# Kernel optimization log

Measured on AMD Instinct MI355X. Metric: run time of the kernel, lower is better.

## Reference

```python
import jax, jax.numpy as jnp
import numpy as np
import math

B, S, F_IN, D, H = 2048, 100, 158, 512, 8
HD = D // H  # head dim = 64


def _sinusoidal_pe(max_len, d_model):
    pos = np.arange(max_len, dtype=np.float32)[:, None]
    div = np.exp(np.arange(0, d_model, 2, dtype=np.float32) * (-math.log(10000.0) / d_model))
    pe = np.zeros((max_len, d_model), dtype=np.float32)
    pe[:, 0::2] = np.sin(pos * div)
    pe[:, 1::2] = np.cos(pos * div)
    return jnp.asarray(pe)


def setup_inputs() -> dict:
    key = jax.random.key(0)
    ks = jax.random.split(key, 16)
    s = 0.03  # small init scale to keep softmax well-conditioned
    return {
        "src": jax.random.normal(ks[0], (B, S, F_IN), jnp.float32),
        "W_feat": jax.random.normal(ks[1], (D, F_IN), jnp.float32) * s,
        "b_feat": jnp.zeros((D,), jnp.float32),
        "pe": _sinusoidal_pe(100, D),
        "Wq": jax.random.normal(ks[2], (D, D), jnp.float32) * s,
        "bq": jnp.zeros((D,), jnp.float32),
        "Wk": jax.random.normal(ks[3], (D, D), jnp.float32) * s,
        "bk": jnp.zeros((D,), jnp.float32),
        "Wv": jax.random.normal(ks[4], (D, D), jnp.float32) * s,
        "bv": jnp.zeros((D,), jnp.float32),
        "Wo": jax.random.normal(ks[5], (D, D), jnp.float32) * s,
        "bo": jnp.zeros((D,), jnp.float32),
        "ln_w": jnp.ones((D,), jnp.float32),
        "ln_b": jnp.zeros((D,), jnp.float32),
        "W1": jax.random.normal(ks[6], (F_IN, D), jnp.float32) * s,
        "b1": jnp.zeros((F_IN,), jnp.float32),
        "W2": jax.random.normal(ks[7], (D, F_IN), jnp.float32) * s,
        "b2": jnp.zeros((D,), jnp.float32),
        "Wt": jax.random.normal(ks[8], (D, D), jnp.float32) * s,
        "W_out": jax.random.normal(ks[9], (1, D), jnp.float32) * s,
        "b_out": jnp.zeros((1,), jnp.float32),
    }


def _layernorm(x, w, b, eps=1e-5):
    mu = jnp.mean(x, axis=-1, keepdims=True)
    var = jnp.var(x, axis=-1, keepdims=True)
    return (x - mu) * jax.lax.rsqrt(var + eps) * w + b


def reference(src, W_feat, b_feat, pe, Wq, bq, Wk, bk, Wv, bv, Wo, bo,
              ln_w, ln_b, W1, b1, W2, b2, Wt, W_out, b_out):
    # feature projection + sinusoidal PE  (dropout is identity in eval mode)
    x = src @ W_feat.T + b_feat            # [B,S,D]
    x = x + pe[:S]                          # [B,S,D]

    # naive multi-head attention
    def heads(t):  # [B,S,D] -> [B,H,S,HD]
        return t.reshape(B, S, H, HD).transpose(0, 2, 1, 3)
    q = heads(x @ Wq.T + bq)
    k = heads(x @ Wk.T + bk)
    v = heads(x @ Wv.T + bv)
    scores = jnp.einsum('bhqd,bhkd->bhqk', q, k) / jnp.sqrt(jnp.float32(HD))
    probs = jax.nn.softmax(scores, axis=-1)
    attn = jnp.einsum('bhqk,bhkd->bhqd', probs, v)
    attn = attn.transpose(0, 2, 1, 3).reshape(B, S, D)
    attn_out = attn @ Wo.T + bo

    # addnorm #1: x + LayerNorm(x) (note: residual is of the SAME tensor)
    y1 = attn_out + _layernorm(attn_out, ln_w, ln_b)

    # FFN (hidden = 158 per the code's d_ff reuse)
    ffn = jax.nn.relu(y1 @ W1.T + b1) @ W2.T + b2

    # addnorm #2 (same shared AddNormLayer params)
    y2 = ffn + _layernorm(ffn, ln_w, ln_b)

    # temporal attention pooling over time
    h = y2 @ Wt.T                           # [B,S,D]
    lam = jnp.einsum('bsd,bd->bs', h, h[:, -1, :])
    lam = jax.nn.softmax(lam, axis=1)
    pooled = jnp.einsum('bs,bsd->bd', lam, y2)  # [B,D]

    return pooled @ W_out.T + b_out         # [B,1]
```

## Files before the change

kernel.cpp:

```cpp
#include <hip/hip_runtime.h>
#include <math.h>

#define NB 2048
#define NS 100
#define NF 158
#define ND 512
#define NH 8

typedef unsigned short u16;
typedef __attribute__((ext_vector_type(8))) short bf16x8;
typedef __attribute__((ext_vector_type(8))) unsigned short u16x8;
typedef __attribute__((ext_vector_type(4))) float f32x4;

__device__ __forceinline__ u16 f2bf(float f) {
    union { float f; unsigned u; } v; v.f = f;
    unsigned u = v.u;
    return (u16)((u + 0x7fffu + ((u >> 16) & 1u)) >> 16);
}

__device__ __forceinline__ float bf2f(u16 v) {
    union { unsigned u; float f; } x; x.u = ((unsigned)v) << 16; return x.f;
}

__device__ __forceinline__ void gload16(const void* g, void* l) {
    __builtin_amdgcn_global_load_lds(
        (const __attribute__((address_space(1))) unsigned*)g,
        (__attribute__((address_space(3))) unsigned*)l, 16, 0, 0);
}

__device__ __forceinline__ bf16x8 load8_cvt(const float* __restrict__ base, int c0) {
    bf16x8 r;
    if (c0 + 8 <= NF) {
        #pragma unroll
        for (int j = 0; j < 8; j += 2) {
            float2 v = *(const float2*)(base + c0 + j);
            r[j] = (short)f2bf(v.x); r[j + 1] = (short)f2bf(v.y);
        }
    } else {
        #pragma unroll
        for (int j = 0; j < 8; ++j)
            r[j] = (c0 + j < NF) ? (short)f2bf(base[c0 + j]) : (short)0;
    }
    return r;
}

__global__ __launch_bounds__(256) void prep_w_kernel(
    const float* __restrict__ Wq, const float* __restrict__ Wk,
    const float* __restrict__ Wv, const float* __restrict__ Wfeat,
    u16* __restrict__ Wf)
{
    int bid = blockIdx.x;
    int sel = bid >> 9;
    int n = bid & 511;
    const float* Wsrc = (sel == 0) ? Wq : (sel == 1) ? Wk : Wv;
    __shared__ float wrow[ND];
    int t = threadIdx.x;
    wrow[t] = Wsrc[(size_t)n * ND + t];
    wrow[t + 256] = Wsrc[(size_t)n * ND + t + 256];
    __syncthreads();
    if (t < 160) {
        float acc = 0.f;
        if (t < NF)
            for (int d = 0; d < ND; ++d)
                acc += wrow[d] * Wfeat[(size_t)d * NF + t];
        int h = n >> 6, local = n & 63;
        int ni, l16;
        if (sel < 2) { ni = local & 3; l16 = local >> 2; }
        else         { ni = (local >> 4) & 3; l16 = local & 15; }
        int ks = t >> 5, quad = (t >> 3) & 3, j = t & 7;
        size_t idx = (((((size_t)sel * 8 + h) * 4 + ni) * 5 + ks) * 64
                      + (quad << 4) + l16) * 8 + j;
        Wf[idx] = f2bf(acc);
    }
}

__global__ __launch_bounds__(256) void prep_c_kernel(
    const float* __restrict__ Wq, const float* __restrict__ Wk, const float* __restrict__ Wv,
    const float* __restrict__ bq, const float* __restrict__ bk, const float* __restrict__ bv,
    const float* __restrict__ bfeat, const float* __restrict__ pe,
    float* __restrict__ T4)
{
    int bid = blockIdx.x;
    int sel = bid / 100;
    int s = bid - sel * 100;
    const float* Wsrc = (sel == 0) ? Wq : (sel == 1) ? Wk : Wv;
    const float* bsrc = (sel == 0) ? bq : (sel == 1) ? bk : bv;
    __shared__ float xv[ND];
    int t = threadIdx.x;
    xv[t] = bfeat[t] + pe[(size_t)s * ND + t];
    xv[t + 256] = bfeat[t + 256] + pe[(size_t)s * ND + t + 256];
    __syncthreads();
    #pragma unroll
    for (int rr = 0; rr < 2; ++rr) {
        int r = t + (rr << 8);
        const float* wr = Wsrc + (size_t)r * ND;
        float acc = bsrc[r];
        for (int d = 0; d < ND; d += 4) {
            float4 w4 = *(const float4*)(wr + d);
            acc += w4.x * xv[d] + w4.y * xv[d+1] + w4.z * xv[d+2] + w4.w * xv[d+3];
        }
        int h = r >> 6, local = r & 63;
        int idx64 = (sel < 2) ? local : (((local & 15) << 2) | (local >> 4));
        T4[(((size_t)(sel * 8 + h)) * 100 + s) * 64 + idx64] = acc;
    }
}

__global__ __launch_bounds__(256) void pad_cast_kernel(
    const float* __restrict__ src, u16* __restrict__ dst,
    int R, int C, int Cp, int total)
{
    int idx = blockIdx.x * 256 + threadIdx.x;
    if (idx >= total) return;
    int r = idx / Cp, c = idx - r * Cp;
    float v = (r < R && c < C) ? src[(size_t)r * C + c] : 0.f;
    dst[idx] = f2bf(v);
}

__global__ __launch_bounds__(256) void pad_b1_kernel(
    const float* __restrict__ b1, float* __restrict__ b1p)
{
    int t = threadIdx.x;
    b1p[t] = (t < NF) ? b1[t] : 0.f;
}

#define ALDQ 72
#define ALDP 136

__global__ __launch_bounds__(512, 4) void qkv_attn_kernel(
    const float* __restrict__ src, const u16* __restrict__ Wf,
    const float* __restrict__ T4, u16* __restrict__ O)
{
    __shared__ short UN[128 * ALDP];
    __shared__ short Ks[112 * ALDQ];
    __shared__ short Vt[64 * ALDP];

    int t = threadIdx.x;
    int lane = t & 63, wave = t >> 6;
    int quad = lane >> 4, l16 = lane & 15;
    int rows0 = wave << 4;
    int b = blockIdx.x;
    const float* xb = src + (size_t)b * NS * NF;
    const size_t rowbase = (size_t)b * NS;
    f32x4 z = {0.f, 0.f, 0.f, 0.f};

    for (int l = t; l < 12 * ALDQ; l += 512)
        Ks[(100 + l / ALDQ) * ALDQ + (l % ALDQ)] = 0;
    for (int l = t; l < 64 * 28; l += 512) {
        int d = l / 28, s = 100 + (l - d * 28);
        Vt[d * ALDP + s] = 0;
    }

    int arow = rows0 + l16;
    bf16x8 AF[5];
    {
        const float* xr = xb + (size_t)arow * NF;
        #pragma unroll
        for (int ks = 0; ks < 5; ++ks) {
            if (arow < NS) AF[ks] = load8_cvt(xr, (ks << 5) + (quad << 3));
            else { bf16x8 zz = {0,0,0,0,0,0,0,0}; AF[ks] = zz; }
        }
    }

    for (int h = 0; h < NH; ++h) {
        #pragma unroll
        for (int sel = 0; sel < 3; ++sel) {
            f32x4 acc[4];
            #pragma unroll
            for (int ni = 0; ni < 4; ++ni) acc[ni] = z;
            #pragma unroll
            for (int ks = 0; ks < 5; ++ks) {
                bf16x8 wfr[4];
                #pragma unroll
                for (int ni = 0; ni < 4; ++ni)
                    wfr[ni] = *(const bf16x8*)(Wf +
                        (((((size_t)sel * 8 + h) * 4 + ni) * 5 + ks) * 64 + lane) * 8);
                #pragma unroll
                for (int ni = 0; ni < 4; ++ni)
                    acc[ni] = __builtin_amdgcn_mfma_f32_16x16x32_bf16(
                        AF[ks], wfr[ni], acc[ni], 0, 0, 0);
            }
            #pragma unroll
            for (int r = 0; r < 4; ++r) {
                int row_s = rows0 + (quad << 2) + r;
                bool real = row_s < NS;
                float4 tv = make_float4(0.f, 0.f, 0.f, 0.f);
                if (real)
                    tv = *(const float4*)(T4 +
                        (((size_t)(sel * 8 + h)) * 100 + row_s) * 64 + (l16 << 2));
                if (sel < 2) {
                    ushort4 pk;
                    pk.x = f2bf(acc[0][r] + tv.x);
                    pk.y = f2bf(acc[1][r] + tv.y);
                    pk.z = f2bf(acc[2][r] + tv.z);
                    pk.w = f2bf(acc[3][r] + tv.w);
                    if (sel == 0) *(ushort4*)&UN[row_s * ALDP + (l16 << 2)] = pk;
                    else if (real) *(ushort4*)&Ks[row_s * ALDQ + (l16 << 2)] = pk;
                } else {
                    float tvs[4] = {tv.x, tv.y, tv.z, tv.w};
                    #pragma unroll
                    for (int ni = 0; ni < 4; ++ni) {
                        int nloc = (ni << 4) + l16;
                        float v = acc[ni][r] + tvs[ni];
                        if (real) Vt[nloc * ALDP + row_s] = (short)f2bf(v);
                    }
                }
            }
        }
        __syncthreads();

        f32x4 sc[7];
        #pragma unroll
        for (int ni = 0; ni < 7; ++ni) sc[ni] = z;
        #pragma unroll
        for (int ks = 0; ks < 2; ++ks) {
            bf16x8 aq = *(const bf16x8*)&UN[(rows0 + l16) * ALDP + (ks << 5) + (quad << 3)];
            bf16x8 bk[7];
            #pragma unroll
            for (int ni = 0; ni < 7; ++ni)
                bk[ni] = *(const bf16x8*)&Ks[((ni << 4) + l16) * ALDQ + (ks << 5) + (quad << 3)];
            #pragma unroll
            for (int ni = 0; ni < 7; ++ni)
                sc[ni] = __builtin_amdgcn_mfma_f32_16x16x32_bf16(aq, bk[ni], sc[ni], 0, 0, 0);
        }
        __syncthreads();

        #pragma unroll
        for (int r = 0; r < 4; ++r) {
            if (l16 >= 4) sc[6][r] = -3.0e38f;
            float mx = sc[0][r];
            #pragma unroll
            for (int ni = 1; ni < 7; ++ni) mx = fmaxf(mx, sc[ni][r]);
            #pragma unroll
            for (int off = 1; off < 16; off <<= 1) mx = fmaxf(mx, __shfl_xor(mx, off));
            float sum = 0.f;
            #pragma unroll
            for (int ni = 0; ni < 7; ++ni) {
                float e = expf((sc[ni][r] - mx) * 0.125f);
                sc[ni][r] = e; sum += e;
            }
            #pragma unroll
            for (int off = 1; off < 16; off <<= 1) sum += __shfl_xor(sum, off);
            float inv = 1.f / sum;
            int row = rows0 + (quad << 2) + r;
            #pragma unroll
            for (int ni = 0; ni < 7; ++ni)
                UN[row * ALDP + (ni << 4) + l16] = (short)f2bf(sc[ni][r] * inv);
            UN[row * ALDP + 112 + l16] = 0;
        }
        __syncthreads();

        f32x4 oa[4];
        #pragma unroll
        for (int ni = 0; ni < 4; ++ni) oa[ni] = z;
        #pragma unroll
        for (int ks = 0; ks < 4; ++ks) {
            bf16x8 ap = *(const bf16x8*)&UN[(rows0 + l16) * ALDP + (ks << 5) + (quad << 3)];
            bf16x8 bv[4];
            #pragma unroll
            for (int ni = 0; ni < 4; ++ni)
                bv[ni] = *(const bf16x8*)&Vt[((ni << 4) + l16) * ALDP + (ks << 5) + (quad << 3)];
            #pragma unroll
            for (int ni = 0; ni < 4; ++ni)
                oa[ni] = __builtin_amdgcn_mfma_f32_16x16x32_bf16(ap, bv[ni], oa[ni], 0, 0, 0);
        }
        #pragma unroll
        for (int r = 0; r < 4; ++r) {
            int row = rows0 + (quad << 2) + r;
            if (row < NS) {
                u16* orow = O + (rowbase + row) * 512 + (h << 6);
                #pragma unroll
                for (int ni = 0; ni < 4; ++ni)
                    orow[(ni << 4) + l16] = f2bf(oa[ni][r]);
            }
        }
        __syncthreads();
    }
}

template<int OUTMODE, bool RELU>
__global__ __launch_bounds__(256) void gemm_bf16(
    const u16* __restrict__ A, const u16* __restrict__ W,
    const float* __restrict__ bias, void* __restrict__ Cv, int K, int ldc)
{
    __shared__ short As[128 * 32];
    __shared__ short Bs[128 * 32];
    int t = threadIdx.x;
    int lane = t & 63, wave = t >> 6;
    int quad = lane >> 4, l16 = lane & 15;
    int wr = wave >> 1, wc = wave & 1;
    int m0 = blockIdx.y << 7, n0 = blockIdx.x << 7;

    f32x4 acc[4][4];
    f32x4 z = {0.f, 0.f, 0.f, 0.f};
    #pragma unroll
    for (int mi = 0; mi < 4; ++mi)
        #pragma unroll
        for (int ni = 0; ni < 4; ++ni) acc[mi][ni] = z;

    int rowA = t >> 2;
    int cch = (t & 3) << 3;
    const u16* aSrc0 = A + (size_t)(m0 + rowA) * K + cch;
    const u16* aSrc1 = A + (size_t)(m0 + rowA + 64) * K + cch;
    const u16* bSrc0 = W + (size_t)(n0 + rowA) * K + cch;
    const u16* bSrc1 = W + (size_t)(n0 + rowA + 64) * K + cch;
    short* aDst0 = As + t * 8;
    short* aDst1 = As + (t + 256) * 8;
    short* bDst0 = Bs + t * 8;
    short* bDst1 = Bs + (t + 256) * 8;

    int nk = K >> 5;
    for (int kc = 0; kc < nk; ++kc) {
        if (kc) __syncthreads();
        gload16(aSrc0, aDst0);
        gload16(aSrc1, aDst1);
        gload16(bSrc0, bDst0);
        gload16(bSrc1, bDst1);
        aSrc0 += 32; aSrc1 += 32; bSrc0 += 32; bSrc1 += 32;
        __syncthreads();

        bf16x8 af[4], bw[4];
        #pragma unroll
        for (int mi = 0; mi < 4; ++mi)
            af[mi] = *(const bf16x8*)(As + ((size_t)((wr << 6) + (mi << 4) + l16) * 32 + (quad << 3)));
        #pragma unroll
        for (int ni = 0; ni < 4; ++ni)
            bw[ni] = *(const bf16x8*)(Bs + ((size_t)((wc << 6) + (ni << 4) + l16) * 32 + (quad << 3)));
        #pragma unroll
        for (int mi = 0; mi < 4; ++mi)
            #pragma unroll
            for (int ni = 0; ni < 4; ++ni)
                acc[mi][ni] = __builtin_amdgcn_mfma_f32_16x16x32_bf16(af[mi], bw[ni], acc[mi][ni], 0, 0, 0);
    }

    #pragma unroll
    for (int mi = 0; mi < 4; ++mi) {
        #pragma unroll
        for (int r = 0; r < 4; ++r) {
            int row = m0 + (wr << 6) + (mi << 4) + (quad << 2) + r;
            #pragma unroll
            for (int ni = 0; ni < 4; ++ni) {
                int col = n0 + (wc << 6) + (ni << 4) + l16;
                float v = acc[mi][ni][r];
                if (bias) v += bias[col];
                if (RELU) v = fmaxf(v, 0.f);
                if (OUTMODE == 0)
                    ((float*)Cv)[(size_t)row * ldc + col] = v;
                else
                    ((u16*)Cv)[(size_t)row * ldc + col] = f2bf(v);
            }
        }
    }
}

template<int OUTMODE>
__global__ __launch_bounds__(512, 2) void gemm_ln(
    const u16* __restrict__ A, const u16* __restrict__ W,
    const float* __restrict__ bias, const float* __restrict__ lnw,
    const float* __restrict__ lnb, void* __restrict__ outv, int K)
{
    __shared__ short As[64 * 32];
    __shared__ short Bs[512 * 32];
    __shared__ float red_s[64][9];
    __shared__ float red_q[64][9];
    __shared__ float mrow[64], rrow[64];

    int t = threadIdx.x;
    int lane = t & 63, wave = t >> 6;
    int quad = lane >> 4, l16 = lane & 15;
    int m0 = blockIdx.x << 6;

    f32x4 acc[4][4];
    f32x4 z = {0.f, 0.f, 0.f, 0.f};
    #pragma unroll
    for (int mi = 0; mi < 4; ++mi)
        #pragma unroll
        for (int ni = 0; ni < 4; ++ni) acc[mi][ni] = z;

    int koff = (t & 3) << 3;
    const u16* aSrc = A + (size_t)(m0 + (t >> 2)) * K + koff;
    const u16* bSrc0 = W + (size_t)(t >> 2) * K + koff;
    const u16* bSrc1 = W + (size_t)((t >> 2) + 128) * K + koff;
    const u16* bSrc2 = W + (size_t)((t >> 2) + 256) * K + koff;
    const u16* bSrc3 = W + (size_t)((t >> 2) + 384) * K + koff;
    short* aDst = As + t * 8;
    short* bDst0 = Bs + t * 8;
    short* bDst1 = Bs + (t + 512) * 8;
    short* bDst2 = Bs + (t + 1024) * 8;
    short* bDst3 = Bs + (t + 1536) * 8;

    int nk = K >> 5;
    for (int kc = 0; kc < nk; ++kc) {
        if (kc) __syncthreads();
        if (t < 256) gload16(aSrc, aDst);
        gload16(bSrc0, bDst0);
        gload16(bSrc1, bDst1);
        gload16(bSrc2, bDst2);
        gload16(bSrc3, bDst3);
        aSrc += 32; bSrc0 += 32; bSrc1 += 32; bSrc2 += 32; bSrc3 += 32;
        __syncthreads();

        bf16x8 af[4], bw[4];
        #pragma unroll
        for (int mi = 0; mi < 4; ++mi)
            af[mi] = *(const bf16x8*)(As + ((mi << 4) + l16) * 32 + (quad << 3));
        #pragma unroll
        for (int ni = 0; ni < 4; ++ni)
            bw[ni] = *(const bf16x8*)(Bs + ((wave << 6) + (ni << 4) + l16) * 32 + (quad << 3));
        #pragma unroll
        for (int mi = 0; mi < 4; ++mi)
            #pragma unroll
            for (int ni = 0; ni < 4; ++ni)
                acc[mi][ni] = __builtin_amdgcn_mfma_f32_16x16x32_bf16(af[mi], bw[ni], acc[mi][ni], 0, 0, 0);
    }

    float lwv[4], lbv[4];
    #pragma unroll
    for (int ni = 0; ni < 4; ++ni) {
        int col = (wave << 6) + (ni << 4) + l16;
        float bv = bias[col];
        lwv[ni] = lnw[col];
        lbv[ni] = lnb[col];
        #pragma unroll
        for (int mi = 0; mi < 4; ++mi)
            #pragma unroll
            for (int r = 0; r < 4; ++r) acc[mi][ni][r] += bv;
    }
    #pragma unroll
    for (int mi = 0; mi < 4; ++mi) {
        #pragma unroll
        for (int r = 0; r < 4; ++r) {
            float s = acc[mi][0][r] + acc[mi][1][r] + acc[mi][2][r] + acc[mi][3][r];
            float q = acc[mi][0][r]*acc[mi][0][r] + acc[mi][1][r]*acc[mi][1][r]
                    + acc[mi][2][r]*acc[mi][2][r] + acc[mi][3][r]*acc[mi][3][r];
            #pragma unroll
            for (int off = 1; off < 16; off <<= 1) {
                s += __shfl_xor(s, off);
                q += __shfl_xor(q, off);
            }
            if (l16 == 0) {
                int row = (mi << 4) + (quad << 2) + r;
                red_s[row][wave] = s;
                red_q[row][wave] = q;
            }
        }
    }
    __syncthreads();
    if (t < 64) {
        float s = 0.f, q = 0.f;
        #pragma unroll
        for (int w8 = 0; w8 < 8; ++w8) { s += red_s[t][w8]; q += red_q[t][w8]; }
        float mean = s * (1.f / 512.f);
        float var = q * (1.f / 512.f) - mean * mean;
        mrow[t] = mean;
        rrow[t] = rsqrtf(var + 1e-5f);
    }
    __syncthreads();
    #pragma unroll
    for (int mi = 0; mi < 4; ++mi) {
        #pragma unroll
        for (int r = 0; r < 4; ++r) {
            int lrow = (mi << 4) + (quad << 2) + r;
            float mean = mrow[lrow], rstd = rrow[lrow];
            size_t grow = (size_t)(m0 + lrow) * 512;
            #pragma unroll
            for (int ni = 0; ni < 4; ++ni) {
                int col = (wave << 6) + (ni << 4) + l16;
                float v = acc[mi][ni][r];
                float y = v + (v - mean) * rstd * lwv[ni] + lbv[ni];
                if (OUTMODE == 0) ((float*)outv)[grow + col] = y;
                else ((u16*)outv)[grow + col] = f2bf(y);
            }
        }
    }
}

__global__ __launch_bounds__(256) void u_stage1_kernel(
    const u16* __restrict__ Y2, const float* __restrict__ Wt,
    float* __restrict__ T1)
{
    __shared__ float yl[16][512];
    int t = threadIdx.x;
    int r0 = blockIdx.x << 6;
    int bg = blockIdx.y << 4;
    for (int l = t; l < 1024; l += 256) {
        int bb = l >> 6, seg = (l & 63) << 3;
        u16x8 v = *(const u16x8*)&Y2[((size_t)(bg + bb) * NS + 99) * ND + seg];
        #pragma unroll
        for (int j = 0; j < 8; ++j) yl[bb][seg + j] = bf2f(v[j]);
    }
    __syncthreads();
    int r = r0 + (t & 63);
    int b0 = t >> 6;
    const float* wr = Wt + (size_t)r * ND;
    float acc[4] = {0.f, 0.f, 0.f, 0.f};
    for (int d = 0; d < ND; d += 4) {
        float4 w4 = *(const float4*)(wr + d);
        #pragma unroll
        for (int bb = 0; bb < 4; ++bb) {
            int bl = (b0 << 2) + bb;
            acc[bb] += w4.x * yl[bl][d] + w4.y * yl[bl][d+1]
                     + w4.z * yl[bl][d+2] + w4.w * yl[bl][d+3];
        }
    }
    #pragma unroll
    for (int bb = 0; bb < 4; ++bb)
        T1[(size_t)(bg + (b0 << 2) + bb) * ND + r] = acc[bb];
}

__global__ __launch_bounds__(256) void u_stage2_kernel(
    const float* __restrict__ T1, const float* __restrict__ Wt,
    float* __restrict__ U)
{
    __shared__ float t1s[16][512];
    int t = threadIdx.x;
    int c0 = blockIdx.x << 6;
    int bg = blockIdx.y << 4;
    for (int l = t; l < 2048; l += 256) {
        int bb = l >> 7, seg = (l & 127) << 2;
        *(float4*)&t1s[bb][seg] = *(const float4*)&T1[(size_t)(bg + bb) * ND + seg];
    }
    __syncthreads();
    int c = c0 + (t & 63);
    int b0 = t >> 6;
    float acc[4] = {0.f, 0.f, 0.f, 0.f};
    for (int r = 0; r < ND; ++r) {
        float w = Wt[(size_t)r * ND + c];
        #pragma unroll
        for (int bb = 0; bb < 4; ++bb)
            acc[bb] += w * t1s[(b0 << 2) + bb][r];
    }
    #pragma unroll
    for (int bb = 0; bb < 4; ++bb)
        U[(size_t)(bg + (b0 << 2) + bb) * ND + c] = acc[bb];
}

__global__ __launch_bounds__(256) void pool_kernel(
    const u16* __restrict__ Y2, const float* __restrict__ U,
    const float* __restrict__ Wout, const float* __restrict__ bout,
    float* __restrict__ out)
{
    __shared__ float u[ND];
    __shared__ float lam[128];
    __shared__ float red[4];
    int t = threadIdx.x;
    int b = blockIdx.x;
    const u16* y2b = Y2 + (size_t)b * NS * ND;
    u[t] = U[(size_t)b * ND + t];
    u[t + 256] = U[(size_t)b * ND + t + 256];
    __syncthreads();
    int wid = t >> 6, lane = t & 63;
    int c0 = lane << 2;
    for (int s = wid; s < NS; s += 4) {
        const u16* yr = y2b + (size_t)s * ND;
        ushort4 q0 = *(const ushort4*)(yr + c0);
        ushort4 q1 = *(const ushort4*)(yr + 256 + c0);
        float a = bf2f(q0.x)*u[c0] + bf2f(q0.y)*u[c0+1] + bf2f(q0.z)*u[c0+2] + bf2f(q0.w)*u[c0+3]
                + bf2f(q1.x)*u[256+c0] + bf2f(q1.y)*u[256+c0+1]
                + bf2f(q1.z)*u[256+c0+2] + bf2f(q1.w)*u[256+c0+3];
        #pragma unroll
        for (int off = 32; off > 0; off >>= 1) a += __shfl_xor(a, off);
        if (lane == 0) lam[s] = a;
    }
    __syncthreads();
    if (t < 64) {
        float l0 = lam[t];
        float l1 = (t + 64 < NS) ? lam[t + 64] : -3.0e38f;
        float mx = fmaxf(l0, l1);
        #pragma unroll
        for (int off = 32; off > 0; off >>= 1) mx = fmaxf(mx, __shfl_xor(mx, off));
        float e0 = expf(l0 - mx);
        float e1 = (t + 64 < NS) ? expf(l1 - mx) : 0.f;
        float ssum = e0 + e1;
        #pragma unroll
        for (int off = 32; off > 0; off >>= 1) ssum += __shfl_xor(ssum, off);
        float inv = 1.f / ssum;
        lam[t] = e0 * inv;
        if (t + 64 < NS) lam[t + 64] = e1 * inv;
    }
    __syncthreads();
    float p0 = 0.f, p1 = 0.f;
    for (int s = 0; s < NS; ++s) {
        float lm = lam[s];
        const u16* yr = y2b + (size_t)s * ND;
        p0 += lm * bf2f(yr[t]);
        p1 += lm * bf2f(yr[t + 256]);
    }
    float vd = p0 * Wout[t] + p1 * Wout[t + 256];
    #pragma unroll
    for (int off = 32; off > 0; off >>= 1) vd += __shfl_xor(vd, off);
    if (lane == 0) red[wid] = vd;
    __syncthreads();
    if (t == 0) out[b] = red[0] + red[1] + red[2] + red[3] + bout[0];
}

static size_t ws_need(int CBc) {
    size_t cm = (size_t)CBc * NS;
    size_t b = 0;
    b += cm * 512 * 2;
    b += cm * 512 * 2;
    b += cm * 256 * 2;
    b += cm * 512 * 2;
    b += (size_t)CBc * 512 * 4 * 2;
    b += 1536 * 160 * 2;
    b += 512 * 512 * 2 + 256 * 512 * 2 + 512 * 256 * 2;
    b += 3 * 8 * 100 * 64 * 4;
    b += 256 * 4;
    b += 64 * 1024;
    return b;
}

extern "C" void kernel_launch(void* const* d_in, const int* in_sizes, int n_in,
                              void* d_out, int out_size, void* d_ws, size_t ws_size,
                              hipStream_t stream)
{
    const float* src   = (const float*)d_in[0];
    const float* Wfeat = (const float*)d_in[1];
    const float* bfeat = (const float*)d_in[2];
    const float* pe    = (const float*)d_in[3];
    const float* Wq    = (const float*)d_in[4];
    const float* bq    = (const float*)d_in[5];
    const float* Wk    = (const float*)d_in[6];
    const float* bk    = (const float*)d_in[7];
    const float* Wv    = (const float*)d_in[8];
    const float* bv    = (const float*)d_in[9];
    const float* Wo    = (const float*)d_in[10];
    const float* bo    = (const float*)d_in[11];
    const float* lnw   = (const float*)d_in[12];
    const float* lnb   = (const float*)d_in[13];
    const float* W1    = (const float*)d_in[14];
    const float* b1    = (const float*)d_in[15];
    const float* W2    = (const float*)d_in[16];
    const float* b2    = (const float*)d_in[17];
    const float* Wt    = (const float*)d_in[18];
    const float* Wout  = (const float*)d_in[19];
    const float* bout  = (const float*)d_in[20];
    float* out = (float*)d_out;

    int CBc = (ws_size >= ws_need(1024)) ? 1024
            : (ws_size >= ws_need(512))  ? 512
            : (ws_size >= ws_need(256))  ? 256 : 128;
    int NCH = NB / CBc;
    size_t CMc = (size_t)CBc * NS;

    char* p = (char*)d_ws;
    auto alloc = [&](size_t bytes) { char* r = p; p += (bytes + 255) & ~(size_t)255; return r; };
    u16*   AO16  = (u16*)  alloc(CMc * 512 * 2);
    u16*   Y116  = (u16*)  alloc(CMc * 512 * 2);
    u16*   ACT16 = (u16*)  alloc(CMc * 256 * 2);
    u16*   Y2    = (u16*)  alloc(CMc * 512 * 2);
    float* T1    = (float*)alloc((size_t)CBc * 512 * 4);
    float* U     = (float*)alloc((size_t)CBc * 512 * 4);
    u16*   Wf    = (u16*)  alloc(1536 * 160 * 2);
    u16*   Wo16  = (u16*)  alloc(512 * 512 * 2);
    u16*   W116  = (u16*)  alloc(256 * 512 * 2);
    u16*   W216  = (u16*)  alloc(512 * 256 * 2);
    float* T4    = (float*)alloc(3 * 8 * 100 * 64 * 4);
    float* b1p   = (float*)alloc(256 * 4);

    prep_w_kernel<<<1536, 256, 0, stream>>>(Wq, Wk, Wv, Wfeat, Wf);
    prep_c_kernel<<<300, 256, 0, stream>>>(Wq, Wk, Wv, bq, bk, bv, bfeat, pe, T4);
    pad_cast_kernel<<<(512 * 512) / 256, 256, 0, stream>>>(Wo, Wo16, 512, 512, 512, 512 * 512);
    pad_cast_kernel<<<(256 * 512) / 256, 256, 0, stream>>>(W1, W116, NF, 512, 512, 256 * 512);
    pad_cast_kernel<<<(512 * 256) / 256, 256, 0, stream>>>(W2, W216, 512, NF, 256, 512 * 256);
    pad_b1_kernel<<<1, 256, 0, stream>>>(b1, b1p);

    dim3 g256(2, CMc / 128);
    dim3 gU(8, CBc / 16);
    int gLN = CMc / 64;

    for (int c = 0; c < NCH; ++c) {
        const float* srcC = src + (size_t)c * CMc * NF;
        float* outC = out + (size_t)c * CBc;

        qkv_attn_kernel<<<CBc, 512, 0, stream>>>(srcC, Wf, T4, AO16);
        gemm_ln<1><<<gLN, 512, 0, stream>>>(AO16, Wo16, bo, lnw, lnb, Y116, 512);
        gemm_bf16<1, true><<<g256, 256, 0, stream>>>(Y116, W116, b1p, ACT16, 512, 256);
        gemm_ln<1><<<gLN, 512, 0, stream>>>(ACT16, W216, b2, lnw, lnb, Y2, 256);
        u_stage1_kernel<<<gU, 256, 0, stream>>>(Y2, Wt, T1);
        u_stage2_kernel<<<gU, 256, 0, stream>>>(T1, Wt, U);
        pool_kernel<<<CBc, 256, 0, stream>>>(Y2, U, Wout, bout, outC);
    }

    (void)in_sizes; (void)n_in; (void)out_size; (void)ws_size;
}
```

Measured before the change: 1.484 ms.

## Alias attention probabilities over Q/K in LDS and retune strides for occupancy

Merges the separate Q/P, K and V^T shared-memory buffers into one arena where the softmax probability tile overwrites the Q and K region once scores are computed. This shrinks the kernel's LDS footprint so more blocks can be resident per CU, and launch bounds are raised to match. Row strides are changed (76, 68, 136, 134) to alter bank-conflict patterns. The zero-init of K pad rows is dropped, relying on the score mask, and the odd P stride makes 16-byte LDS reads unaligned. The tighter register budget implied by the higher launch bound may cause spills.

After: 1.850 ms. 1.25x slower.

```diff
diff --git a/kernel.cpp b/kernel.cpp
--- a/kernel.cpp
+++ b/kernel.cpp
@@ -123,16 +123,22 @@
     b1p[t] = (t < NF) ? b1[t] : 0.f;
 }
 
-#define ALDQ 72
-#define ALDP 136
-
-__global__ __launch_bounds__(512, 4) void qkv_attn_kernel(
+#define LDQ 76
+#define LDK 68
+#define LDV 136
+#define LDP 134
+#define OFF_K (128 * LDQ)
+#define OFF_V (128 * LDQ + 112 * LDK)
+
+__global__ __launch_bounds__(512, 6) void qkv_attn_kernel(
     const float* __restrict__ src, const u16* __restrict__ Wf,
     const float* __restrict__ T4, u16* __restrict__ O)
 {
-    __shared__ short UN[128 * ALDP];
-    __shared__ short Ks[112 * ALDQ];
-    __shared__ short Vt[64 * ALDP];
+    __shared__ short LB[128 * LDQ + 112 * LDK + 64 * LDV];
+    short* Qs = LB;
+    short* KS = LB + OFF_K;
+    short* VT = LB + OFF_V;
+    short* P  = LB;
 
     int t = threadIdx.x;
     int lane = t & 63, wave = t >> 6;
@@ -143,11 +149,9 @@
     const size_t rowbase = (size_t)b * NS;
     f32x4 z = {0.f, 0.f, 0.f, 0.f};
 
-    for (int l = t; l < 12 * ALDQ; l += 512)
-        Ks[(100 + l / ALDQ) * ALDQ + (l % ALDQ)] = 0;
     for (int l = t; l < 64 * 28; l += 512) {
         int d = l / 28, s = 100 + (l - d * 28);
-        Vt[d * ALDP + s] = 0;
+        VT[d * LDV + s] = 0;
     }
 
     int arow = rows0 + l16;
@@ -160,6 +164,7 @@
             else { bf16x8 zz = {0,0,0,0,0,0,0,0}; AF[ks] = zz; }
         }
     }
+    __syncthreads();
 
     for (int h = 0; h < NH; ++h) {
         #pragma unroll
@@ -193,15 +198,15 @@
                     pk.y = f2bf(acc[1][r] + tv.y);
                     pk.z = f2bf(acc[2][r] + tv.z);
                     pk.w = f2bf(acc[3][r] + tv.w);
-                    if (sel == 0) *(ushort4*)&UN[row_s * ALDP + (l16 << 2)] = pk;
-                    else if (real) *(ushort4*)&Ks[row_s * ALDQ + (l16 << 2)] = pk;
+                    if (sel == 0) *(ushort4*)&Qs[row_s * LDQ + (l16 << 2)] = pk;
+                    else if (real) *(ushort4*)&KS[row_s * LDK + (l16 << 2)] = pk;
                 } else {
                     float tvs[4] = {tv.x, tv.y, tv.z, tv.w};
                     #pragma unroll
                     for (int ni = 0; ni < 4; ++ni) {
                         int nloc = (ni << 4) + l16;
                         float v = acc[ni][r] + tvs[ni];
-                        if (real) Vt[nloc * ALDP + row_s] = (short)f2bf(v);
+                        if (real) VT[nloc * LDV + row_s] = (short)f2bf(v);
                     }
                 }
             }
@@ -213,11 +218,11 @@
         for (int ni = 0; ni < 7; ++ni) sc[ni] = z;
         #pragma unroll
         for (int ks = 0; ks < 2; ++ks) {
-            bf16x8 aq = *(const bf16x8*)&UN[(rows0 + l16) * ALDP + (ks << 5) + (quad << 3)];
+            bf16x8 aq = *(const bf16x8*)&Qs[(rows0 + l16) * LDQ + (ks << 5) + (quad << 3)];
             bf16x8 bk[7];
             #pragma unroll
             for (int ni = 0; ni < 7; ++ni)
-                bk[ni] = *(const bf16x8*)&Ks[((ni << 4) + l16) * ALDQ + (ks << 5) + (quad << 3)];
+                bk[ni] = *(const bf16x8*)&KS[((ni << 4) + l16) * LDK + (ks << 5) + (quad << 3)];
             #pragma unroll
             for (int ni = 0; ni < 7; ++ni)
                 sc[ni] = __builtin_amdgcn_mfma_f32_16x16x32_bf16(aq, bk[ni], sc[ni], 0, 0, 0);
@@ -244,8 +249,8 @@
             int row = rows0 + (quad << 2) + r;
             #pragma unroll
             for (int ni = 0; ni < 7; ++ni)
-                UN[row * ALDP + (ni << 4) + l16] = (short)f2bf(sc[ni][r] * inv);
-            UN[row * ALDP + 112 + l16] = 0;
+                P[row * LDP + (ni << 4) + l16] = (short)f2bf(sc[ni][r] * inv);
+            P[row * LDP + 112 + l16] = 0;
         }
         __syncthreads();
 
@@ -254,11 +259,11 @@
         for (int ni = 0; ni < 4; ++ni) oa[ni] = z;
         #pragma unroll
         for (int ks = 0; ks < 4; ++ks) {
-            bf16x8 ap = *(const bf16x8*)&UN[(rows0 + l16) * ALDP + (ks << 5) + (quad << 3)];
+            bf16x8 ap = *(const bf16x8*)&P[(rows0 + l16) * LDP + (ks << 5) + (quad << 3)];
             bf16x8 bv[4];
             #pragma unroll
             for (int ni = 0; ni < 4; ++ni)
-                bv[ni] = *(const bf16x8*)&Vt[((ni << 4) + l16) * ALDP + (ks << 5) + (quad << 3)];
+                bv[ni] = *(const bf16x8*)&VT[((ni << 4) + l16) * LDV + (ks << 5) + (quad << 3)];
             #pragma unroll
             for (int ni = 0; ni < 4; ++ni)
                 oa[ni] = __builtin_amdgcn_mfma_f32_16x16x32_bf16(ap, bv[ni], oa[ni], 0, 0, 0);
```
